# Kernel optimization log

Hardware: AMD Instinct MI355X
Metric: run time of the kernel (lower is better)

The kernel has to match this reference:

```python
import jax, jax.numpy as jnp
import numpy as np

N_NODES = 50000
N_EDGES = 600000
D = 128


def _mlp(x, Wa, ba, Wb, bb):
    # 2-layer MLP: Linear -> ReLU -> Linear
    h = jax.nn.relu(x @ Wa + ba)
    return h @ Wb + bb


def _gin_layer(h, src, dst, Wa, ba, Wb, bb):
    # GINConv (sum aggregator, eps=0): apply_func(h + sum_{j in N(i)} h_j)
    agg = jax.ops.segment_sum(h[src], dst, num_segments=N_NODES)
    return _mlp(h + agg, Wa, ba, Wb, bb)


def setup_inputs() -> dict:
    key = jax.random.key(0)
    ks = jax.random.split(key, 8)
    s = 1.0 / np.sqrt(D)
    return {
        "inputs": jax.random.normal(ks[0], (N_NODES, D), dtype=jnp.float32),
        "src": jax.random.randint(ks[1], (N_EDGES,), 0, N_NODES, dtype=jnp.int32),
        "dst": jax.random.randint(ks[2], (N_EDGES,), 0, N_NODES, dtype=jnp.int32),
        "W1a": jax.random.normal(ks[3], (D, D), dtype=jnp.float32) * s,
        "b1a": jnp.zeros((D,), dtype=jnp.float32),
        "W1b": jax.random.normal(ks[4], (D, D), dtype=jnp.float32) * s,
        "b1b": jnp.zeros((D,), dtype=jnp.float32),
        "W2a": jax.random.normal(ks[5], (D, D), dtype=jnp.float32) * s,
        "b2a": jnp.zeros((D,), dtype=jnp.float32),
        "W2b": jax.random.normal(ks[6], (D, D), dtype=jnp.float32) * s,
        "b2b": jnp.zeros((D,), dtype=jnp.float32),
    }


def reference(inputs, src, dst, W1a, b1a, W1b, b1b, W2a, b2a, W2b, b2b):
    h = _gin_layer(inputs, src, dst, W1a, b1a, W1b, b1b)
    h = jax.nn.relu(h)
    h = _gin_layer(h, src, dst, W2a, b2a, W2b, b2b)
    return h
```

## Files before the change

kernel.cpp:

```cpp
#include <hip/hip_runtime.h>
#include <hip/hip_bf16.h>
#include <stdint.h>

#define N_NODES 50000
#define N_EDGES 600000
#define D 128
#define BM 16
#define NBLK (N_NODES / BM)
#define CAP 64
#define DUMMY N_NODES

typedef __attribute__((ext_vector_type(8))) short bf16x8_t;
typedef __attribute__((ext_vector_type(8))) ushort ushort8_t;
typedef __attribute__((ext_vector_type(4))) float f32x4;

__device__ __forceinline__ float bf2f(ushort u) {
    union { uint32_t u; float f; } v;
    v.u = ((uint32_t)u) << 16;
    return v.f;
}
__device__ __forceinline__ ushort f2bf(float f) {
    union { float f; uint32_t u; } v; v.f = f;
    uint32_t u = v.u;
    return (ushort)((u + 0x7fffu + ((u >> 16) & 1u)) >> 16);
}


__global__ __launch_bounds__(256) void init_kernel(int* __restrict__ cur,
                                                   ushort* __restrict__ ibuf,
                                                   ushort* __restrict__ hbuf) {
    int i = blockIdx.x * 256 + threadIdx.x;
    if (i < N_NODES) cur[i] = i << 6;
    if (i < D) {
        ibuf[(size_t)DUMMY * D + i] = 0;
        hbuf[(size_t)DUMMY * D + i] = 0;
    }
}


__global__ __launch_bounds__(256) void scatter_prep(const int* __restrict__ src,
                                                    const int* __restrict__ dst,
                                                    int* __restrict__ cur,
                                                    ushort* __restrict__ csr,
                                                    const float* __restrict__ in,
                                                    ushort* __restrict__ ibuf,
                                                    const float* __restrict__ W1a,
                                                    const float* __restrict__ W1b,
                                                    const float* __restrict__ W2a,
                                                    const float* __restrict__ W2b,
                                                    ushort* __restrict__ wbuf) {
    int tid = blockIdx.x * 256 + threadIdx.x;
    int stride = gridDim.x * 256;
    for (int e = tid; e < N_EDGES; e += stride) {
        int d = dst[e];
        int slot = atomicAdd(&cur[d], 1);
        csr[slot] = (ushort)src[e];
    }
    const int total4 = N_NODES * 32;
    for (int i = tid; i < total4; i += stride) {
        float4 v = ((const float4*)in)[i];
        ushort4 o;
        o.x = f2bf(v.x); o.y = f2bf(v.y); o.z = f2bf(v.z); o.w = f2bf(v.w);
        ((ushort4*)ibuf)[i] = o;
    }
    for (int idx = tid; idx < 65536; idx += stride) {
        const float* srcs[4] = {W1a, W1b, W2a, W2b};
        int mat = idx >> 14;
        int n = (idx >> 7) & 127;
        int k = idx & 127;
        wbuf[idx] = f2bf(srcs[mat][k * 128 + n]);
    }
}


template <int OUT_BF16>
__global__ __launch_bounds__(256) void gin_layer(const ushort* __restrict__ h,
                                                 const int* __restrict__ cur,
                                                 const ushort* __restrict__ csr,
                                                 const ushort* __restrict__ Wat,
                                                 const float* __restrict__ ba,
                                                 const ushort* __restrict__ Wbt,
                                                 const float* __restrict__ bb,
                                                 void* __restrict__ outp) {
    __shared__ ushort xs[BM][136];
    __shared__ ushort hs[BM][136];
    int tid = threadIdx.x;
    int row0 = blockIdx.x * BM;

    {
        int r = tid >> 4;
        int q = tid & 15;
        int row = row0 + r;
        const ushort* hq = h + q * 8;
        float acc[8];
        {
            bf16x8_t t0 = *(const bf16x8_t*)(hq + (size_t)row * D);
            #pragma unroll
            for (int j = 0; j < 8; ++j) acc[j] = bf2f((ushort)t0[j]);
        }
        int sbase = row << 6;
        int n = cur[row] - sbase;
        const ushort* cp = csr + sbase;
        int full = n >> 3;
        int rem = n & 7;
        ushort8_t ii = *(const ushort8_t*)cp;
        for (int it = 0; it < full; ++it) {
            ushort8_t ci = ii;
            int nx = (it + 1 < full) ? (it + 1) * 8 : it * 8;
            ii = *(const ushort8_t*)(cp + nx);
            bf16x8_t g0 = *(const bf16x8_t*)(hq + (size_t)ci[0] * D);
            bf16x8_t g1 = *(const bf16x8_t*)(hq + (size_t)ci[1] * D);
            bf16x8_t g2 = *(const bf16x8_t*)(hq + (size_t)ci[2] * D);
            bf16x8_t g3 = *(const bf16x8_t*)(hq + (size_t)ci[3] * D);
            bf16x8_t g4 = *(const bf16x8_t*)(hq + (size_t)ci[4] * D);
            bf16x8_t g5 = *(const bf16x8_t*)(hq + (size_t)ci[5] * D);
            bf16x8_t g6 = *(const bf16x8_t*)(hq + (size_t)ci[6] * D);
            bf16x8_t g7 = *(const bf16x8_t*)(hq + (size_t)ci[7] * D);
            #pragma unroll
            for (int j = 0; j < 8; ++j) {
                acc[j] += ((bf2f((ushort)g0[j]) + bf2f((ushort)g1[j]))
                         + (bf2f((ushort)g2[j]) + bf2f((ushort)g3[j])))
                        + ((bf2f((ushort)g4[j]) + bf2f((ushort)g5[j]))
                         + (bf2f((ushort)g6[j]) + bf2f((ushort)g7[j])));
            }
        }
        {
            ushort8_t ci = *(const ushort8_t*)(cp + full * 8);
            int idx[8];
            #pragma unroll
            for (int j = 0; j < 8; ++j) idx[j] = (j < rem) ? (int)ci[j] : DUMMY;
            bf16x8_t g0 = *(const bf16x8_t*)(hq + (size_t)idx[0] * D);
            bf16x8_t g1 = *(const bf16x8_t*)(hq + (size_t)idx[1] * D);
            bf16x8_t g2 = *(const bf16x8_t*)(hq + (size_t)idx[2] * D);
            bf16x8_t g3 = *(const bf16x8_t*)(hq + (size_t)idx[3] * D);
            bf16x8_t g4 = *(const bf16x8_t*)(hq + (size_t)idx[4] * D);
            bf16x8_t g5 = *(const bf16x8_t*)(hq + (size_t)idx[5] * D);
            bf16x8_t g6 = *(const bf16x8_t*)(hq + (size_t)idx[6] * D);
            bf16x8_t g7 = *(const bf16x8_t*)(hq + (size_t)idx[7] * D);
            #pragma unroll
            for (int j = 0; j < 8; ++j) {
                acc[j] += ((bf2f((ushort)g0[j]) + bf2f((ushort)g1[j]))
                         + (bf2f((ushort)g2[j]) + bf2f((ushort)g3[j])))
                        + ((bf2f((ushort)g4[j]) + bf2f((ushort)g5[j]))
                         + (bf2f((ushort)g6[j]) + bf2f((ushort)g7[j])));
            }
        }
        bf16x8_t o0;
        #pragma unroll
        for (int j = 0; j < 8; ++j) o0[j] = (short)f2bf(acc[j]);
        *(bf16x8_t*)&xs[r][q * 8] = o0;
    }
    __syncthreads();

    int w = tid >> 6;
    int l = tid & 63;
    int lr = l & 15;
    int g = l >> 4;
    int ch = w * 32;

    {
        bf16x8_t a[4];
        #pragma unroll
        for (int c = 0; c < 4; ++c)
            a[c] = *(const bf16x8_t*)&xs[lr][32 * c + 8 * g];

        #pragma unroll
        for (int nt = 0; nt < 2; ++nt) {
            int col = ch + 16 * nt + lr;
            f32x4 c4 = {0.f, 0.f, 0.f, 0.f};
            const ushort* wrow = Wat + (size_t)col * D + g * 8;
            #pragma unroll
            for (int c = 0; c < 4; ++c) {
                bf16x8_t b = *(const bf16x8_t*)(wrow + 32 * c);
                c4 = __builtin_amdgcn_mfma_f32_16x16x32_bf16(a[c], b, c4, 0, 0, 0);
            }
            float bv = ba[col];
            #pragma unroll
            for (int r = 0; r < 4; ++r) {
                float v = fmaxf(c4[r] + bv, 0.f);
                hs[g * 4 + r][col] = f2bf(v);
            }
        }
    }
    __syncthreads();

    {
        bf16x8_t a2[4];
        #pragma unroll
        for (int c = 0; c < 4; ++c)
            a2[c] = *(const bf16x8_t*)&hs[lr][32 * c + 8 * g];

        #pragma unroll
        for (int nt = 0; nt < 2; ++nt) {
            int col = ch + 16 * nt + lr;
            f32x4 c4 = {0.f, 0.f, 0.f, 0.f};
            const ushort* wrow = Wbt + (size_t)col * D + g * 8;
            #pragma unroll
            for (int c = 0; c < 4; ++c) {
                bf16x8_t b = *(const bf16x8_t*)(wrow + 32 * c);
                c4 = __builtin_amdgcn_mfma_f32_16x16x32_bf16(a2[c], b, c4, 0, 0, 0);
            }
            float bv = bb[col];
            #pragma unroll
            for (int r = 0; r < 4; ++r) {
                int row = row0 + g * 4 + r;
                float v = c4[r] + bv;
                if (OUT_BF16) {
                    xs[g * 4 + r][col] = f2bf(fmaxf(v, 0.f));
                } else {
                    ((float*)outp)[(size_t)row * D + col] = v;
                }
            }
        }
    }
    if (OUT_BF16) {
        __syncthreads();
        int rr = tid >> 4;
        int qq = tid & 15;
        *(bf16x8_t*)((ushort*)outp + (size_t)(row0 + rr) * D + qq * 8) =
            *(const bf16x8_t*)&xs[rr][qq * 8];
    }
}


extern "C" void kernel_launch(void* const* d_in, const int* in_sizes, int n_in,
                              void* d_out, int out_size, void* d_ws, size_t ws_size,
                              hipStream_t stream) {
    const float* inputs = (const float*)d_in[0];
    const int* src = (const int*)d_in[1];
    const int* dst = (const int*)d_in[2];
    const float* W1a = (const float*)d_in[3];
    const float* b1a = (const float*)d_in[4];
    const float* W1b = (const float*)d_in[5];
    const float* b1b = (const float*)d_in[6];
    const float* W2a = (const float*)d_in[7];
    const float* b2a = (const float*)d_in[8];
    const float* W2b = (const float*)d_in[9];
    const float* b2b = (const float*)d_in[10];
    float* out = (float*)d_out;

    int* cur = (int*)d_ws;
    ushort* csr = (ushort*)(cur + N_NODES);
    ushort* wbuf = (ushort*)(((uintptr_t)(csr + (size_t)N_NODES * CAP + 64) + 255)
                             & ~(uintptr_t)255);
    ushort* W1at = wbuf;
    ushort* W1bt = wbuf + 16384;
    ushort* W2at = wbuf + 2 * 16384;
    ushort* W2bt = wbuf + 3 * 16384;
    ushort* ibuf = wbuf + 4 * 16384;
    ushort* hbuf = ibuf + (size_t)(N_NODES + 1) * D;

    init_kernel<<<(N_NODES + 255) / 256, 256, 0, stream>>>(cur, ibuf, hbuf);
    scatter_prep<<<2048, 256, 0, stream>>>(src, dst, cur, csr, inputs, ibuf,
                                           W1a, W1b, W2a, W2b, wbuf);

    gin_layer<1><<<NBLK, 256, 0, stream>>>(ibuf, cur, csr,
                                           W1at, b1a, W1bt, b1b, (void*)hbuf);
    gin_layer<0><<<NBLK, 256, 0, stream>>>(hbuf, cur, csr,
                                           W2at, b2a, W2bt, b2b, (void*)out);
}
```

Measured before the change: 132.9 us.

## Build CSR via two-pass bucketed scatter to localize atomics and writes

```diff
diff --git a/kernel.cpp b/kernel.cpp
--- a/kernel.cpp
+++ b/kernel.cpp
@@ -9,6 +9,8 @@
 #define NBLK (N_NODES / BM)
 #define CAP 64
 #define DUMMY N_NODES
+#define NBUCK 391
+#define BCAP 2048
 
 typedef __attribute__((ext_vector_type(8))) short bf16x8_t;
 typedef __attribute__((ext_vector_type(8))) ushort ushort8_t;
@@ -26,11 +28,11 @@
 }
 
 
-__global__ __launch_bounds__(256) void init_kernel(int* __restrict__ cur,
+__global__ __launch_bounds__(256) void init_kernel(int* __restrict__ bkt_cnt,
                                                    ushort* __restrict__ ibuf,
                                                    ushort* __restrict__ hbuf) {
     int i = blockIdx.x * 256 + threadIdx.x;
-    if (i < N_NODES) cur[i] = i << 6;
+    if (i < NBUCK) bkt_cnt[i] = 0;
     if (i < D) {
         ibuf[(size_t)DUMMY * D + i] = 0;
         hbuf[(size_t)DUMMY * D + i] = 0;
@@ -40,8 +42,8 @@
 
 __global__ __launch_bounds__(256) void scatter_prep(const int* __restrict__ src,
                                                     const int* __restrict__ dst,
-                                                    int* __restrict__ cur,
-                                                    ushort* __restrict__ csr,
+                                                    int* __restrict__ bkt_cnt,
+                                                    uint32_t* __restrict__ bkt,
                                                     const float* __restrict__ in,
                                                     ushort* __restrict__ ibuf,
                                                     const float* __restrict__ W1a,
@@ -53,8 +55,9 @@
     int stride = gridDim.x * 256;
     for (int e = tid; e < N_EDGES; e += stride) {
         int d = dst[e];
-        int slot = atomicAdd(&cur[d], 1);
-        csr[slot] = (ushort)src[e];
+        int b = d >> 7;
+        int slot = atomicAdd(&bkt_cnt[b], 1);
+        bkt[((size_t)b << 11) + slot] = (uint32_t)src[e] | ((uint32_t)(d & 127) << 16);
     }
     const int total4 = N_NODES * 32;
     for (int i = tid; i < total4; i += stride) {
@@ -70,6 +73,30 @@
         int k = idx & 127;
         wbuf[idx] = f2bf(srcs[mat][k * 128 + n]);
     }
+}
+
+
+__global__ __launch_bounds__(256) void bucket2csr(const int* __restrict__ bkt_cnt,
+                                                  const uint32_t* __restrict__ bkt,
+                                                  ushort* __restrict__ csr,
+                                                  int* __restrict__ cur) {
+    __shared__ int cnt[128];
+    int tid = threadIdx.x;
+    int bid = blockIdx.x;
+    int base = bid << 7;
+    if (tid < 128) cnt[tid] = 0;
+    __syncthreads();
+    int n = bkt_cnt[bid];
+    const uint32_t* bp = bkt + ((size_t)bid << 11);
+    for (int i = tid; i < n; i += 256) {
+        uint32_t e = bp[i];
+        int dl = e >> 16;
+        int s = atomicAdd(&cnt[dl], 1);
+        csr[((size_t)(base + dl) << 6) + s] = (ushort)(e & 0xffffu);
+    }
+    __syncthreads();
+    if (tid < 128 && base + tid < N_NODES)
+        cur[base + tid] = ((base + tid) << 6) + cnt[tid];
 }
 
 
@@ -240,7 +267,10 @@
     float* out = (float*)d_out;
 
     int* cur = (int*)d_ws;
-    ushort* csr = (ushort*)(cur + N_NODES);
+    int* bkt_cnt = cur + N_NODES;
+    uint32_t* bkt = (uint32_t*)(((uintptr_t)(bkt_cnt + NBUCK) + 255)
+                                & ~(uintptr_t)255);
+    ushort* csr = (ushort*)(bkt + (size_t)NBUCK * BCAP);
     ushort* wbuf = (ushort*)(((uintptr_t)(csr + (size_t)N_NODES * CAP + 64) + 255)
                              & ~(uintptr_t)255);
     ushort* W1at = wbuf;
@@ -250,9 +280,10 @@
     ushort* ibuf = wbuf + 4 * 16384;
     ushort* hbuf = ibuf + (size_t)(N_NODES + 1) * D;
 
-    init_kernel<<<(N_NODES + 255) / 256, 256, 0, stream>>>(cur, ibuf, hbuf);
-    scatter_prep<<<2048, 256, 0, stream>>>(src, dst, cur, csr, inputs, ibuf,
+    init_kernel<<<2, 256, 0, stream>>>(bkt_cnt, ibuf, hbuf);
+    scatter_prep<<<2048, 256, 0, stream>>>(src, dst, bkt_cnt, bkt, inputs, ibuf,
                                            W1a, W1b, W2a, W2b, wbuf);
+    bucket2csr<<<NBUCK, 256, 0, stream>>>(bkt_cnt, bkt, csr, cur);
 
     gin_layer<1><<<NBLK, 256, 0, stream>>>(ibuf, cur, csr,
                                            W1at, b1a, W1bt, b1b, (void*)hbuf);
```

New measurement: 313.7 us. 136% more time.
